# Performance work log

Hardware: AMD Instinct MI355X
Metric: run time of the kernel (lower is better)

The kernel has to match this reference:

```python
import jax, jax.numpy as jnp
import numpy as np
from jax import lax

# ConvTranspose2d(stride=1, padding=p) == conv with spatially-flipped, in/out-swapped
# weight and padding k-1-p per side. Here k=3, p=1 -> conv padding (1,1).
K = 3
P = 1
_CONV_PAD = K - 1 - P  # = 1

def _rconv(a, w):
    # a: [N,C,H,Wf] real, w: [O,I,kH,kW]
    return lax.conv_general_dilated(
        a, w, window_strides=(1, 1),
        padding=[(_CONV_PAD, _CONV_PAD), (_CONV_PAD, _CONV_PAD)],
        dimension_numbers=("NCHW", "OIHW", "NCHW"))


def setup_inputs() -> dict:
    key = jax.random.key(0)
    k1, k2, k3, k4, k5 = jax.random.split(key, 5)
    N, C_IN, C_OUT, H, W = 8, 16, 16, 512, 512
    x = jax.random.normal(k1, (N, C_IN, H, W), dtype=jnp.float32)
    # torch ConvTranspose2d weight layout: (in, out, kH, kW), complex64 split into re/im
    scale = 1.0 / np.sqrt(C_IN * K * K)
    w_real = jax.random.normal(k2, (C_IN, C_OUT, K, K), dtype=jnp.float32) * scale
    w_imag = jax.random.normal(k3, (C_IN, C_OUT, K, K), dtype=jnp.float32) * scale
    b_real = jax.random.normal(k4, (C_OUT,), dtype=jnp.float32) * scale
    b_imag = jax.random.normal(k5, (C_OUT,), dtype=jnp.float32) * scale
    return {"x": x, "w_real": w_real, "w_imag": w_imag, "b_real": b_real, "b_imag": b_imag}


def reference(x, w_real, w_imag, b_real, b_imag):
    # rfftn over last two dims (norm='backward')
    X = jnp.fft.rfftn(x, axes=(-2, -1), norm="backward")  # [N,C,H,W//2+1] complex64
    Xr, Xi = jnp.real(X), jnp.imag(X)
    # convert transpose-conv weight to equivalent conv weight: flip spatial, swap in/out
    wr = jnp.transpose(jnp.flip(w_real, axis=(-2, -1)), (1, 0, 2, 3))
    wi = jnp.transpose(jnp.flip(w_imag, axis=(-2, -1)), (1, 0, 2, 3))
    # complex conv via real/imag decomposition
    Yr = _rconv(Xr, wr) - _rconv(Xi, wi) + b_real[:, None, None]
    Yi = _rconv(Xr, wi) + _rconv(Xi, wr) + b_imag[:, None, None]
    Y = lax.complex(Yr, Yi)
    # irfftn with no explicit s: last dim -> 2*(Wf-1) = W
    return jnp.fft.irfftn(Y, axes=(-2, -1), norm="backward")
```

## Files before the change

kernel.cpp:

```cpp
#include <hip/hip_runtime.h>
#include <math.h>

#define PI_F 3.14159265358979323846f

#define FI(i) ((i) + ((i) >> 4))
#define TSTRIDE 546

__device__ inline float2 cmulf(float2 a, float2 b) {
    return make_float2(a.x * b.x - a.y * b.y, a.x * b.y + a.y * b.x);
}
__device__ inline float2 cadd(float2 a, float2 b) { return make_float2(a.x + b.x, a.y + b.y); }
__device__ inline float2 csub(float2 a, float2 b) { return make_float2(a.x - b.x, a.y - b.y); }

__device__ inline void cmac(float2& a, float2 w, float2 v) {
    a.x = fmaf(w.x, v.x, a.x);
    a.x = fmaf(-w.y, v.y, a.x);
    a.y = fmaf(w.x, v.y, a.y);
    a.y = fmaf(w.y, v.x, a.y);
}

__device__ inline int xcd_remap(int bid, int q) {
    return (bid & 7) * q + (bid >> 3);
}

__device__ inline void wave_fence() {
    asm volatile("s_waitcnt lgkmcnt(0)" ::: "memory");
    __builtin_amdgcn_sched_barrier(0);
}

template <bool INV>
__device__ inline float2 rot90(float2 z) {
    return INV ? make_float2(-z.y, z.x) : make_float2(z.y, -z.x);
}

template <bool INV>
__device__ inline void dft8(float2 v[8]) {
    const float R2 = 0.70710678118654752f;
    float2 t0 = cadd(v[0], v[4]), t1 = csub(v[0], v[4]);
    float2 t2 = cadd(v[2], v[6]), t3 = csub(v[2], v[6]);
    float2 s0 = cadd(v[1], v[5]), s1 = csub(v[1], v[5]);
    float2 s2 = cadd(v[3], v[7]), s3 = csub(v[3], v[7]);
    float2 rt3 = rot90<INV>(t3), rs3 = rot90<INV>(s3);
    float2 E0 = cadd(t0, t2), E1 = cadd(t1, rt3), E2 = csub(t0, t2), E3 = csub(t1, rt3);
    float2 O0 = cadd(s0, s2), O1 = cadd(s1, rs3), O2 = csub(s0, s2), O3 = csub(s1, rs3);
    float2 rO1 = rot90<INV>(O1), rO2 = rot90<INV>(O2), rO3 = rot90<INV>(O3);
    float2 a1 = make_float2(R2 * (O1.x + rO1.x), R2 * (O1.y + rO1.y));
    float2 a2 = rO2;
    float2 a3 = make_float2(R2 * (rO3.x - O3.x), R2 * (rO3.y - O3.y));
    v[0] = cadd(E0, O0); v[4] = csub(E0, O0);
    v[1] = cadd(E1, a1); v[5] = csub(E1, a1);
    v[2] = cadd(E2, a2); v[6] = csub(E2, a2);
    v[3] = cadd(E3, a3); v[7] = csub(E3, a3);
}

__device__ inline void twiddle8(float2 v[8], float2 w1) {
    float2 w2 = cmulf(w1, w1);
    float2 w3 = cmulf(w2, w1);
    float2 w4 = cmulf(w2, w2);
    float2 w5 = cmulf(w4, w1);
    float2 w6 = cmulf(w3, w3);
    float2 w7 = cmulf(w4, w3);
    v[1] = cmulf(v[1], w1); v[2] = cmulf(v[2], w2); v[3] = cmulf(v[3], w3);
    v[4] = cmulf(v[4], w4); v[5] = cmulf(v[5], w5); v[6] = cmulf(v[6], w6);
    v[7] = cmulf(v[7], w7);
}

template <bool INV>
__device__ inline void fft512_wave_ip(float2 v[8], float2* R, int lane) {
    const float sg = INV ? (6.2831853071795865f / 512.0f)
                         : (-6.2831853071795865f / 512.0f);
    float2 w1;
    __sincosf(sg * (float)lane, &w1.y, &w1.x);
    dft8<INV>(v);
    twiddle8(v, w1);
#pragma unroll
    for (int m = 0; m < 8; ++m) R[FI(8 * lane + m)] = v[m];
    wave_fence();
#pragma unroll
    for (int j = 0; j < 8; ++j) v[j] = R[FI(lane + 64 * j)];
    float2 w1b;
    w1b.x = __shfl(w1.x, lane & 56);
    w1b.y = __shfl(w1.y, lane & 56);
    dft8<INV>(v);
    twiddle8(v, w1b);
    {
        int ob = (lane & 7) + ((lane >> 3) << 6);
#pragma unroll
        for (int m = 0; m < 8; ++m) R[FI(ob + 8 * m)] = v[m];
    }
    wave_fence();
#pragma unroll
    for (int j = 0; j < 8; ++j) v[j] = R[FI(lane + 64 * j)];
    dft8<INV>(v);
}

__global__ __launch_bounds__(256) void k_row_rfft(const float* __restrict__ x,
                                                  float2* __restrict__ G) {
    __shared__ float2 lds[4][544];
    int lane = threadIdx.x & 63;
    int w = threadIdx.x >> 6;
    int pair = blockIdx.x * 4 + w;
    const float* x0 = x + (size_t)(2 * pair) * 512;
    const float* x1 = x0 + 512;
    float2 v[8];
#pragma unroll
    for (int j = 0; j < 8; ++j)
        v[j] = make_float2(x0[lane + 64 * j], x1[lane + 64 * j]);
    fft512_wave_ip<false>(v, lds[w], lane);
    float2 P[5];
#pragma unroll
    for (int m = 0; m < 5; ++m) {
        int src = (64 - lane) & 63;
        float2 p;
        p.x = __shfl(v[7 - m].x, src);
        p.y = __shfl(v[7 - m].y, src);
        if (lane == 0) p = v[(8 - m) & 7];
        P[m] = p;
    }
    float2* g0 = G + (size_t)(2 * pair) * 257;
    float2* g1 = g0 + 257;
#pragma unroll
    for (int m = 0; m < 4; ++m) {
        int k = lane + 64 * m;
        float2 Z = v[m], Pc = P[m];
        float2 S = make_float2(0.5f * (Z.x + Pc.x), 0.5f * (Z.y - Pc.y));
        float2 D = make_float2(Z.x - Pc.x, Z.y + Pc.y);
        float2 T = make_float2(0.5f * D.y, -0.5f * D.x);
        g0[k] = S;
        g1[k] = T;
    }
    if (lane == 0) {
        float2 Z = v[4], Pc = P[4];
        g0[256] = make_float2(0.5f * (Z.x + Pc.x), 0.5f * (Z.y - Pc.y));
        float2 D = make_float2(Z.x - Pc.x, Z.y + Pc.y);
        g1[256] = make_float2(0.5f * D.y, -0.5f * D.x);
    }
}

__global__ __launch_bounds__(1024) void k_col_fft(const float2* __restrict__ G,
                                                  float2* __restrict__ XT) {
    __shared__ float2 tile[16][TSTRIDE];
    int tid = threadIdx.x;
    int l = xcd_remap(blockIdx.x, 272);
    int nc = l / 17;
    int v0 = (l % 17) * 16;
#pragma unroll
    for (int j = 0; j < 8; ++j) {
        int e = tid + 1024 * j;
        int dv = e & 15, h = e >> 4;
        int v = v0 + dv;
        float2 val = make_float2(0.0f, 0.0f);
        if (v < 257) val = G[((size_t)nc * 512 + h) * 257 + v];
        tile[dv][FI(h)] = val;
    }
    __syncthreads();
    int lane = tid & 63, w = tid >> 6;
    float2* R = tile[w];
    float2 vv[8];
#pragma unroll
    for (int j = 0; j < 8; ++j) vv[j] = R[FI(lane + 64 * j)];
    fft512_wave_ip<false>(vv, R, lane);
    int v = v0 + w;
    if (v < 257) {
        float2* dst = XT + ((size_t)nc * 257 + v) * 512;
#pragma unroll
        for (int m = 0; m < 8; ++m) dst[lane + 64 * m] = vv[m];
    }
}

__global__ __launch_bounds__(256, 8) void k_conv(const float2* __restrict__ XT,
                                                 float2* __restrict__ YT,
                                                 const float* __restrict__ wr,
                                                 const float* __restrict__ wi,
                                                 const float* __restrict__ br,
                                                 const float* __restrict__ bi) {
    __shared__ float2 Xs[8 * 4 * 66];
    int tid = threadIdx.x;
    int bid = blockIdx.x;
    int ut = bid & 7;
    int rest = bid >> 3;
    int vt = rest % 129;
    int n = rest / 129;
    int u0 = ut * 64;
    int v0 = vt * 2;

    int lane = tid & 63;
    int wv = __builtin_amdgcn_readfirstlane(tid >> 6);
    int o0 = wv * 4;

    float2 acc[2][4];
#pragma unroll
    for (int oo = 0; oo < 4; ++oo) {
        float2 bv = make_float2(br[o0 + oo], bi[o0 + oo]);
        acc[0][oo] = bv;
        acc[1][oo] = bv;
    }

    for (int half = 0; half < 2; ++half) {
        if (half) __syncthreads();
        for (int l = tid; l < 2112; l += 256) {
            int c = l / 264;
            int rem = l - c * 264;
            int dvr = rem / 66;
            int uu = rem - dvr * 66;
            int vg = v0 - 1 + dvr;
            int ug = u0 - 1 + uu;
            int cg = half * 8 + c;
            float2 val = make_float2(0.0f, 0.0f);
            if (vg >= 0 && vg < 257 && ug >= 0 && ug < 512)
                val = XT[(((size_t)n * 16 + cg) * 257 + vg) * 512 + ug];
            Xs[l] = val;
        }
        __syncthreads();

        for (int c = 0; c < 8; ++c) {
            int cg = half * 8 + c;
            float2 xv[4][3];
#pragma unroll
            for (int dvr = 0; dvr < 4; ++dvr) {
                const float2* row = &Xs[(c * 4 + dvr) * 66];
                xv[dvr][0] = row[lane];
                xv[dvr][1] = row[lane + 1];
                xv[dvr][2] = row[lane + 2];
            }
#pragma unroll
            for (int oo = 0; oo < 4; ++oo) {
                const float* wrp = wr + ((size_t)(cg * 16 + o0 + oo)) * 9;
                const float* wip = wi + ((size_t)(cg * 16 + o0 + oo)) * 9;
                float wre[9], wim[9];
#pragma unroll
                for (int t = 0; t < 9; ++t) { wre[t] = wrp[t]; wim[t] = wip[t]; }
#pragma unroll
                for (int kw = 0; kw < 3; ++kw) {
#pragma unroll
                    for (int kh = 0; kh < 3; ++kh) {
                        int t = kh * 3 + kw;
                        int xj = 2 - kh;
                        float2 w = make_float2(wre[t], wim[t]);
                        cmac(acc[0][oo], w, xv[2 - kw][xj]);
                        cmac(acc[1][oo], w, xv[3 - kw][xj]);
                    }
                }
            }
        }
    }

#pragma unroll
    for (int oo = 0; oo < 4; ++oo) {
#pragma unroll
        for (int vv = 0; vv < 2; ++vv) {
            int v = v0 + vv;
            if (v < 257)
                YT[(((size_t)n * 16 + o0 + oo) * 257 + v) * 512 + u0 + lane] =
                    acc[vv][oo];
        }
    }
}

__global__ __launch_bounds__(256) void k_col_ifft(const float2* __restrict__ YT,
                                                  float2* __restrict__ ZT) {
    __shared__ float2 lds[4][544];
    int lane = threadIdx.x & 63;
    int w = threadIdx.x >> 6;
    int no = blockIdx.x / 65;
    int v = (blockIdx.x % 65) * 4 + w;
    if (v >= 257) return;
    const float2* src = YT + ((size_t)no * 257 + v) * 512;
    float2 vv[8];
#pragma unroll
    for (int j = 0; j < 8; ++j) vv[j] = src[lane + 64 * j];
    fft512_wave_ip<true>(vv, lds[w], lane);
    const float sc = 1.0f / 512.0f;
    float2* dst = ZT + ((size_t)no * 257 + v) * 512;
#pragma unroll
    for (int m = 0; m < 8; ++m)
        dst[lane + 64 * m] = make_float2(vv[m].x * sc, vv[m].y * sc);
}

__global__ __launch_bounds__(512) void k_row_irfft(const float2* __restrict__ ZT,
                                                   float* __restrict__ out) {
    __shared__ float2 tile[16][TSTRIDE];
    int tid = threadIdx.x;
    int no = blockIdx.x >> 5;
    int h0 = (blockIdx.x & 31) * 16;
#pragma unroll
    for (int j = 0; j < 9; ++j) {
        int e = tid + 512 * j;
        if (e < 4112) {
            int dh = e & 15, vv = e >> 4;
            tile[dh][FI(vv)] = ZT[((size_t)no * 257 + vv) * 512 + h0 + dh];
        }
    }
    __syncthreads();
    int lane = tid & 63, w = tid >> 6;
    float2* Ra = tile[2 * w];
    float2* Rb = tile[2 * w + 1];
    float2 v[8];
#pragma unroll
    for (int m = 0; m < 8; ++m) {
        int i = lane + 64 * m;
        float2 a, b, W;
        if (i <= 256) {
            a = Ra[FI(i)];
            b = Rb[FI(i)];
            if (i == 0 || i == 256) { a.y = 0.0f; b.y = 0.0f; }
            W = make_float2(a.x - b.y, a.y + b.x);
        } else {
            int ii = 512 - i;
            a = Ra[FI(ii)];
            b = Rb[FI(ii)];
            W = make_float2(a.x + b.y, -a.y + b.x);
        }
        v[m] = W;
    }
    fft512_wave_ip<true>(v, Ra, lane);
    const float sc = 1.0f / 512.0f;
    float* d0 = out + ((size_t)no * 512 + h0 + 2 * w) * 512;
    float* d1 = d0 + 512;
#pragma unroll
    for (int m = 0; m < 8; ++m) {
        d0[lane + 64 * m] = v[m].x * sc;
        d1[lane + 64 * m] = v[m].y * sc;
    }
}

extern "C" void kernel_launch(void* const* d_in, const int* in_sizes, int n_in,
                              void* d_out, int out_size, void* d_ws, size_t ws_size,
                              hipStream_t stream) {
    const float* x  = (const float*)d_in[0];
    const float* wr = (const float*)d_in[1];
    const float* wi = (const float*)d_in[2];
    const float* br = (const float*)d_in[3];
    const float* bi = (const float*)d_in[4];
    float* out = (float*)d_out;

    const size_t bufElems = (size_t)128 * 257 * 512;
    float2* A = (float2*)d_ws;
    float2* B = A + bufElems;

    k_row_rfft<<<8192, 256, 0, stream>>>(x, A);
    k_col_fft<<<128 * 17, 1024, 0, stream>>>(A, B);
    k_conv<<<8 * 129 * 8, 256, 0, stream>>>(B, A, wr, wi, br, bi);
    k_col_ifft<<<128 * 65, 256, 0, stream>>>(A, B);
    k_row_irfft<<<128 * 32, 512, 0, stream>>>(B, out);
}
```

Measured before the change: 593.4 us.

## Fuse complex conv with column inverse FFT in one kernel

Merges the spectral-domain conv and the column inverse FFT into one kernel. Each block now handles a full 512-length column for one (n, v) and computes all 16 output channels per thread, then runs the inverse FFT on the results through shared memory. This drops one full global round trip of the intermediate spectrum and one launch. The cost is 16 accumulators per thread, fewer and larger blocks (2056 blocks of 512 threads), and more redundant per-thread weight loads, which could lower occupancy.

```diff
diff --git a/kernel.cpp b/kernel.cpp
--- a/kernel.cpp
+++ b/kernel.cpp
@@ -168,65 +168,53 @@
     }
 }
 
-__global__ __launch_bounds__(256, 8) void k_conv(const float2* __restrict__ XT,
-                                                 float2* __restrict__ YT,
-                                                 const float* __restrict__ wr,
-                                                 const float* __restrict__ wi,
-                                                 const float* __restrict__ br,
-                                                 const float* __restrict__ bi) {
-    __shared__ float2 Xs[8 * 4 * 66];
+__global__ __launch_bounds__(512, 6) void k_conv_ifft(const float2* __restrict__ XT,
+                                                      float2* __restrict__ ZT,
+                                                      const float* __restrict__ wr,
+                                                      const float* __restrict__ wi,
+                                                      const float* __restrict__ br,
+                                                      const float* __restrict__ bi) {
+    __shared__ float2 smem[4 * 3 * 516];
     int tid = threadIdx.x;
-    int bid = blockIdx.x;
-    int ut = bid & 7;
-    int rest = bid >> 3;
-    int vt = rest % 129;
-    int n = rest / 129;
-    int u0 = ut * 64;
-    int v0 = vt * 2;
-
-    int lane = tid & 63;
-    int wv = __builtin_amdgcn_readfirstlane(tid >> 6);
-    int o0 = wv * 4;
-
-    float2 acc[2][4];
-#pragma unroll
-    for (int oo = 0; oo < 4; ++oo) {
-        float2 bv = make_float2(br[o0 + oo], bi[o0 + oo]);
-        acc[0][oo] = bv;
-        acc[1][oo] = bv;
-    }
-
-    for (int half = 0; half < 2; ++half) {
-        if (half) __syncthreads();
-        for (int l = tid; l < 2112; l += 256) {
-            int c = l / 264;
-            int rem = l - c * 264;
-            int dvr = rem / 66;
-            int uu = rem - dvr * 66;
-            int vg = v0 - 1 + dvr;
-            int ug = u0 - 1 + uu;
-            int cg = half * 8 + c;
+    int l = xcd_remap(blockIdx.x, 257);
+    int v = l % 257;
+    int n = l / 257;
+
+    float2 acc[16];
+#pragma unroll
+    for (int o = 0; o < 16; ++o)
+        acc[o] = make_float2(br[o], bi[o]);
+
+    for (int cg = 0; cg < 4; ++cg) {
+        __syncthreads();
+        for (int s = tid; s < 6168; s += 512) {
+            int c = s / 1542;
+            int rem = s - c * 1542;
+            int dv = rem / 514;
+            int uu = rem - dv * 514;
+            int vg = v - 1 + dv;
+            int ug = uu - 1;
             float2 val = make_float2(0.0f, 0.0f);
             if (vg >= 0 && vg < 257 && ug >= 0 && ug < 512)
-                val = XT[(((size_t)n * 16 + cg) * 257 + vg) * 512 + ug];
-            Xs[l] = val;
+                val = XT[(((size_t)n * 16 + cg * 4 + c) * 257 + vg) * 512 + ug];
+            smem[(c * 3 + dv) * 516 + uu] = val;
         }
         __syncthreads();
 
-        for (int c = 0; c < 8; ++c) {
-            int cg = half * 8 + c;
-            float2 xv[4][3];
-#pragma unroll
-            for (int dvr = 0; dvr < 4; ++dvr) {
-                const float2* row = &Xs[(c * 4 + dvr) * 66];
-                xv[dvr][0] = row[lane];
-                xv[dvr][1] = row[lane + 1];
-                xv[dvr][2] = row[lane + 2];
+        for (int c = 0; c < 4; ++c) {
+            int cgc = cg * 4 + c;
+            float2 xv[3][3];
+#pragma unroll
+            for (int dv = 0; dv < 3; ++dv) {
+                const float2* row = &smem[(c * 3 + dv) * 516];
+                xv[dv][0] = row[tid];
+                xv[dv][1] = row[tid + 1];
+                xv[dv][2] = row[tid + 2];
             }
 #pragma unroll
-            for (int oo = 0; oo < 4; ++oo) {
-                const float* wrp = wr + ((size_t)(cg * 16 + o0 + oo)) * 9;
-                const float* wip = wi + ((size_t)(cg * 16 + o0 + oo)) * 9;
+            for (int o = 0; o < 16; ++o) {
+                const float* wrp = wr + ((size_t)(cgc * 16 + o)) * 9;
+                const float* wip = wi + ((size_t)(cgc * 16 + o)) * 9;
                 float wre[9], wim[9];
 #pragma unroll
                 for (int t = 0; t < 9; ++t) { wre[t] = wrp[t]; wim[t] = wip[t]; }
@@ -235,46 +223,33 @@
 #pragma unroll
                     for (int kh = 0; kh < 3; ++kh) {
                         int t = kh * 3 + kw;
-                        int xj = 2 - kh;
                         float2 w = make_float2(wre[t], wim[t]);
-                        cmac(acc[0][oo], w, xv[2 - kw][xj]);
-                        cmac(acc[1][oo], w, xv[3 - kw][xj]);
+                        cmac(acc[o], w, xv[2 - kw][2 - kh]);
                     }
                 }
             }
         }
     }
 
-#pragma unroll
-    for (int oo = 0; oo < 4; ++oo) {
-#pragma unroll
-        for (int vv = 0; vv < 2; ++vv) {
-            int v = v0 + vv;
-            if (v < 257)
-                YT[(((size_t)n * 16 + o0 + oo) * 257 + v) * 512 + u0 + lane] =
-                    acc[vv][oo];
-        }
-    }
-}
-
-__global__ __launch_bounds__(256) void k_col_ifft(const float2* __restrict__ YT,
-                                                  float2* __restrict__ ZT) {
-    __shared__ float2 lds[4][544];
-    int lane = threadIdx.x & 63;
-    int w = threadIdx.x >> 6;
-    int no = blockIdx.x / 65;
-    int v = (blockIdx.x % 65) * 4 + w;
-    if (v >= 257) return;
-    const float2* src = YT + ((size_t)no * 257 + v) * 512;
-    float2 vv[8];
-#pragma unroll
-    for (int j = 0; j < 8; ++j) vv[j] = src[lane + 64 * j];
-    fft512_wave_ip<true>(vv, lds[w], lane);
+    int lane = tid & 63;
+    int wvid = tid >> 6;
     const float sc = 1.0f / 512.0f;
-    float2* dst = ZT + ((size_t)no * 257 + v) * 512;
-#pragma unroll
-    for (int m = 0; m < 8; ++m)
-        dst[lane + 64 * m] = make_float2(vv[m].x * sc, vv[m].y * sc);
+    for (int r = 0; r < 2; ++r) {
+        __syncthreads();
+#pragma unroll
+        for (int k = 0; k < 8; ++k)
+            smem[k * 544 + FI(tid)] = acc[r * 8 + k];
+        __syncthreads();
+        float2* R = smem + wvid * 544;
+        float2 vv[8];
+#pragma unroll
+        for (int j = 0; j < 8; ++j) vv[j] = R[FI(lane + 64 * j)];
+        fft512_wave_ip<true>(vv, R, lane);
+        float2* dst = ZT + (((size_t)n * 16 + r * 8 + wvid) * 257 + v) * 512;
+#pragma unroll
+        for (int m = 0; m < 8; ++m)
+            dst[lane + 64 * m] = make_float2(vv[m].x * sc, vv[m].y * sc);
+    }
 }
 
 __global__ __launch_bounds__(512) void k_row_irfft(const float2* __restrict__ ZT,
@@ -340,7 +315,6 @@
 
     k_row_rfft<<<8192, 256, 0, stream>>>(x, A);
     k_col_fft<<<128 * 17, 1024, 0, stream>>>(A, B);
-    k_conv<<<8 * 129 * 8, 256, 0, stream>>>(B, A, wr, wi, br, bi);
-    k_col_ifft<<<128 * 65, 256, 0, stream>>>(A, B);
-    k_row_irfft<<<128 * 32, 512, 0, stream>>>(B, out);
-}
+    k_conv_ifft<<<8 * 257, 512, 0, stream>>>(B, A, wr, wi, br, bi);
+    k_row_irfft<<<128 * 32, 512, 0, stream>>>(A, out);
+}
```

After: 682.4 us. 15.0% more time.
